# Performance work log

Hardware: AMD Instinct MI355X
Metric: run time of the kernel (lower is better)

The kernel has to match this reference:

```python
import jax, jax.numpy as jnp
import numpy as np

B, T, S, SYM, FFT = 256, 4, 2, 14, 128   # batch, num_tx, streams_per_tx, ofdm symbols, fft size
NSC, GUARD = 108, 10                      # effective subcarriers, guard offset
L = SYM * NSC                             # 1512, de-mash matrix dimension


def setup_inputs() -> dict:
    key = jax.random.key(0)
    k1, k2, k3, k4 = jax.random.split(key, 4)
    scale = 1.0 / np.sqrt(L).astype(np.float32)  # keep C roughly unitary-scaled
    return {
        "x_real": jax.random.normal(k1, (B, T, S, SYM, FFT), jnp.float32),
        "x_imag": jax.random.normal(k2, (B, T, S, SYM, FFT), jnp.float32),
        "C_real": jax.random.normal(k3, (L, L), jnp.float32) * scale,
        "C_imag": jax.random.normal(k4, (L, L), jnp.float32) * scale,
        "sc_ind": jnp.arange(NSC, dtype=jnp.int32) + GUARD,  # effective subcarrier indices
    }


def reference(x_real, x_imag, C_real, C_imag, sc_ind):
    # Complex RG and de-mash matrix
    x = jax.lax.complex(x_real, x_imag)           # [B,T,S,SYM,FFT] complex64
    C = jax.lax.complex(C_real, C_imag)           # [L,L] complex64

    # gather effective subcarriers along last axis
    y = jnp.take(x, sc_ind, axis=-1)              # [B,T,S,SYM,NSC]
    b, t, s, sym, nsc = y.shape

    # flatten_last_dims(y, 2) and multiply from right by C^H (adjoint=True)
    yf = y.reshape(b, t, s, sym * nsc)            # [B,T,S,L]
    yf = jnp.einsum('btsl,ml->btsm', yf, jnp.conj(C))  # y @ C^H
    y = yf.reshape(b, t, s, sym, nsc)             # [B,T,S,SYM,NSC]

    # scatter back into the full grid (equivalent to the transpose/scatter_nd/transpose chain,
    # since sc_ind is unique and the scatter is along the subcarrier axis)
    out = jnp.zeros(x.shape, x.dtype).at[..., sc_ind].set(y)

    # return real/imag stacked so the output is a single float32 array
    return jnp.stack([out.real, out.imag], axis=0)  # [2,B,T,S,SYM,FFT]
```

## Files before the change

kernel.cpp:

```cpp
#include <hip/hip_runtime.h>
#include <cstdint>
#include <cstddef>


typedef _Float16 half_t;
typedef half_t half8 __attribute__((ext_vector_type(8)));
typedef half_t half4 __attribute__((ext_vector_type(4)));
typedef half_t half2_t __attribute__((ext_vector_type(2)));
typedef float floatx4 __attribute__((ext_vector_type(4)));
typedef float floatv4 __attribute__((ext_vector_type(4)));

#define M_DIM 2048
#define K_DIM 3072
#define L_PAD 1536
#define N2_DIM 1536
#define LDIM 1512
#define NSC 108
#define SYMS 14
#define FFT 128
#define ROWLEN (SYMS * FFT)

#define BM 64
#define BN 64
#define BK 64
#define NITER (L_PAD / BK)

#define PA2_BLOCKS 6048
#define PW2_BLOCKS 4608
#define PAP_BLOCKS 48
#define PG_BLOCKS 4480
#define PREP_BLOCKS (PA2_BLOCKS + PW2_BLOCKS + PAP_BLOCKS + PG_BLOCKS)

typedef __attribute__((address_space(3))) uint32_t lds_u32_t;
typedef const __attribute__((address_space(1))) uint32_t glob_u32_t;

__device__ __forceinline__ void gl2lds16(const void* g, void* l) {
    __builtin_amdgcn_global_load_lds((glob_u32_t*)g, (lds_u32_t*)l, 16, 0, 0);
}

__global__ __launch_bounds__(256) void prep_all(
    const float* __restrict__ xr, const float* __restrict__ xi,
    const float* __restrict__ Cr, const float* __restrict__ Ci,
    const int* __restrict__ sc,
    half_t* __restrict__ A, half_t* __restrict__ W, float* __restrict__ out)
{
    const int b = blockIdx.x;
    const int t = threadIdx.x;

    if (b < PA2_BLOCKS) {
        int idx = b * 256 + t;
        int jp = idx % 54;
        int rest = idx / 54;
        int sym = rest % 14;
        int row = rest / 14;
        int s0 = sc[2 * jp];
        int s1 = sc[2 * jp + 1];
        const float* xrp = xr + (size_t)row * ROWLEN + sym * FFT;
        const float* xip = xi + (size_t)row * ROWLEN + sym * FFT;
        half2_t hr = { (half_t)xrp[s0], (half_t)xrp[s1] };
        half2_t hi = { (half_t)xip[s0], (half_t)xip[s1] };
        size_t dst = (size_t)row * K_DIM + sym * NSC + 2 * jp;
        *(half2_t*)(A + dst) = hr;
        *(half2_t*)(A + dst + L_PAD) = hi;
    } else if (b < PA2_BLOCKS + PW2_BLOCKS) {
        int idx = (b - PA2_BLOCKS) * 256 + t;
        int kq = idx % 768;
        int n = idx / 768;
        int k0 = kq * 4;
        floatv4 f = {0.0f, 0.0f, 0.0f, 0.0f};
        if (n < LDIM) {
            if (k0 < L_PAD) {
                if (k0 < LDIM)
                    f = *(const floatv4*)(Cr + (size_t)n * LDIM + k0);
            } else {
                int l = k0 - L_PAD;
                if (l < LDIM)
                    f = *(const floatv4*)(Ci + (size_t)n * LDIM + l);
            }
        }
        half4 h = { (half_t)f.x, (half_t)f.y, (half_t)f.z, (half_t)f.w };
        *(half4*)(W + (size_t)n * K_DIM + k0) = h;
    } else if (b < PA2_BLOCKS + PW2_BLOCKS + PAP_BLOCKS) {
        int idx = (b - PA2_BLOCKS - PW2_BLOCKS) * 256 + t;
        int c = idx % 6;
        int row = idx / 6;
        int col = (c < 3) ? (LDIM + c * 8) : (L_PAD + LDIM + (c - 3) * 8);
        half8 z = {};
        *(half8*)(A + (size_t)row * K_DIM + col) = z;
    } else {
        int idx = (b - PA2_BLOCKS - PW2_BLOCKS - PAP_BLOCKS) * 256 + t;
        int c20 = idx % 20;
        int rest = idx / 20;
        int sym = rest % 14;
        int rowri = rest / 14;
        int col = (c20 < 10) ? c20 : (NSC + c20);
        out[(size_t)rowri * ROWLEN + sym * FFT + col] = 0.0f;
    }
}

__global__ __launch_bounds__(256, 3) void gemm_scatter(
    const half_t* __restrict__ A,
    const half_t* __restrict__ W,
    const int* __restrict__ sc,
    float* __restrict__ out)
{
    __shared__ __align__(16) half_t As[BM * 2 * BK];
    __shared__ __align__(16) half_t Ws[BN * 2 * BK];

    const int t = threadIdx.x;
    const int bn = blockIdx.x;
    const int bm = blockIdx.y;
    const int lane = t & 63;
    const int w = t >> 6;
    const int wm = (w >> 1) * 32;
    const int wn = (w & 1) * 32;

    floatx4 aRR[2][2] = {}, aII[2][2] = {}, aIR[2][2] = {}, aRI[2][2] = {};

    const half_t* gA[4];
    const half_t* gW[4];
    half_t* lA[4];
    half_t* lW[4];
#pragma unroll
    for (int r = 0; r < 4; ++r) {
        int c = r * 256 + t;
        int row = c >> 4, slot = c & 15;
        int g = slot ^ (row & 15);
        int gcol = (g < 8) ? g * 8 : (L_PAD + (g - 8) * 8);
        gA[r] = A + (size_t)(bm * BM + row) * K_DIM + gcol;
        lA[r] = As + c * 8;
        gW[r] = W + (size_t)(bn * BN + row) * K_DIM + gcol;
        lW[r] = Ws + c * 8;
    }

    const int fr = lane & 15;
    const int cr = lane >> 4;

    for (int kb = 0; kb < NITER; ++kb) {
        __syncthreads();
#pragma unroll
        for (int r = 0; r < 4; ++r) gl2lds16(gA[r], lA[r]);
#pragma unroll
        for (int r = 0; r < 4; ++r) gl2lds16(gW[r], lW[r]);
#pragma unroll
        for (int r = 0; r < 4; ++r) { gA[r] += BK; gW[r] += BK; }
        __syncthreads();

#pragma unroll
        for (int ss = 0; ss < 2; ++ss) {
            const int sR = ((ss * 4 + cr) ^ fr) * 8;
            const int sI = ((8 + ss * 4 + cr) ^ fr) * 8;
            half8 yr[2], yi[2], cR[2], cI[2];
#pragma unroll
            for (int i = 0; i < 2; ++i) {
                int rb = (wm + i * 16 + fr) * (2 * BK);
                yr[i] = *(const half8*)&As[rb + sR];
                yi[i] = *(const half8*)&As[rb + sI];
            }
#pragma unroll
            for (int j = 0; j < 2; ++j) {
                int rb = (wn + j * 16 + fr) * (2 * BK);
                cR[j] = *(const half8*)&Ws[rb + sR];
                cI[j] = *(const half8*)&Ws[rb + sI];
            }
#pragma unroll
            for (int i = 0; i < 2; ++i)
#pragma unroll
                for (int j = 0; j < 2; ++j) {
                    aRR[i][j] = __builtin_amdgcn_mfma_f32_16x16x32_f16(
                        yr[i], cR[j], aRR[i][j], 0, 0, 0);
                    aII[i][j] = __builtin_amdgcn_mfma_f32_16x16x32_f16(
                        yi[i], cI[j], aII[i][j], 0, 0, 0);
                    aIR[i][j] = __builtin_amdgcn_mfma_f32_16x16x32_f16(
                        yi[i], cR[j], aIR[i][j], 0, 0, 0);
                    aRI[i][j] = __builtin_amdgcn_mfma_f32_16x16x32_f16(
                        yr[i], cI[j], aRI[i][j], 0, 0, 0);
                }
        }
    }

    const int rq = lane >> 4;
#pragma unroll
    for (int j = 0; j < 2; ++j) {
        int n = bn * BN + wn + j * 16 + fr;
        if (n >= LDIM) continue;
        int sym = n / NSC;
        int jj = n - sym * NSC;
        size_t colR = (size_t)sym * FFT + sc[jj];
        size_t colI = (size_t)M_DIM * ROWLEN + colR;
#pragma unroll
        for (int i = 0; i < 2; ++i) {
            int m0 = bm * BM + wm + i * 16 + rq * 4;
#pragma unroll
            for (int r = 0; r < 4; ++r) {
                float vr = aRR[i][j][r] + aII[i][j][r];
                float vi = aIR[i][j][r] - aRI[i][j][r];
                out[colR + (size_t)(m0 + r) * ROWLEN] = vr;
                out[colI + (size_t)(m0 + r) * ROWLEN] = vi;
            }
        }
    }
}

extern "C" void kernel_launch(void* const* d_in, const int* in_sizes, int n_in,
                              void* d_out, int out_size, void* d_ws, size_t ws_size,
                              hipStream_t stream) {
    const float* xr = (const float*)d_in[0];
    const float* xi = (const float*)d_in[1];
    const float* Cr = (const float*)d_in[2];
    const float* Ci = (const float*)d_in[3];
    const int* sc   = (const int*)d_in[4];
    float* out = (float*)d_out;

    half_t* Ah = (half_t*)d_ws;
    half_t* Wh = (half_t*)((char*)d_ws + (size_t)M_DIM * K_DIM * 2);

    prep_all<<<PREP_BLOCKS, 256, 0, stream>>>(
        xr, xi, Cr, Ci, sc, Ah, Wh, out);

    dim3 grid(N2_DIM / BN, M_DIM / BM);
    gemm_scatter<<<grid, 256, 0, stream>>>(Ah, Wh, sc, out);
}
```

Before: 144.7 us.

## Double-buffer GEMM LDS tiles with 2-wave blocks and halved K step

Restructures the complex GEMM main loop to double-buffer LDS. The next K tile is prefetched via global_load_lds while MFMAs run on the current one, and only one barrier is kept per iteration. Blocks shrink from 4 to 2 waves, each wave computing a 32x64 tile with more accumulators, and BK drops to 32 with a matching 8-slot XOR swizzle. This hides global load latency, at the cost of fewer waves per block, higher register pressure and twice as many loop iterations.

```diff
diff --git a/kernel.cpp b/kernel.cpp
--- a/kernel.cpp
+++ b/kernel.cpp
@@ -22,7 +22,7 @@
 
 #define BM 64
 #define BN 64
-#define BK 64
+#define BK 32
 #define NITER (L_PAD / BK)
 
 #define PA2_BLOCKS 6048
@@ -98,91 +98,95 @@
     }
 }
 
-__global__ __launch_bounds__(256, 3) void gemm_scatter(
+__global__ __launch_bounds__(128, 2) void gemm_scatter(
     const half_t* __restrict__ A,
     const half_t* __restrict__ W,
     const int* __restrict__ sc,
     float* __restrict__ out)
 {
-    __shared__ __align__(16) half_t As[BM * 2 * BK];
-    __shared__ __align__(16) half_t Ws[BN * 2 * BK];
+    __shared__ __align__(16) half_t As[2][BM * 2 * BK];
+    __shared__ __align__(16) half_t Ws[2][BN * 2 * BK];
 
     const int t = threadIdx.x;
     const int bn = blockIdx.x;
     const int bm = blockIdx.y;
     const int lane = t & 63;
     const int w = t >> 6;
-    const int wm = (w >> 1) * 32;
-    const int wn = (w & 1) * 32;
-
-    floatx4 aRR[2][2] = {}, aII[2][2] = {}, aIR[2][2] = {}, aRI[2][2] = {};
+    const int wm = w * 32;
+
+    floatx4 aRR[2][4] = {}, aII[2][4] = {}, aIR[2][4] = {}, aRI[2][4] = {};
 
     const half_t* gA[4];
     const half_t* gW[4];
-    half_t* lA[4];
-    half_t* lW[4];
+    int lOff[4];
 #pragma unroll
     for (int r = 0; r < 4; ++r) {
-        int c = r * 256 + t;
-        int row = c >> 4, slot = c & 15;
-        int g = slot ^ (row & 15);
-        int gcol = (g < 8) ? g * 8 : (L_PAD + (g - 8) * 8);
+        int c = r * 128 + t;
+        int row = c >> 3, slot = c & 7;
+        int g = slot ^ (row & 7);
+        int gcol = (g < 4) ? g * 8 : (L_PAD + (g - 4) * 8);
         gA[r] = A + (size_t)(bm * BM + row) * K_DIM + gcol;
-        lA[r] = As + c * 8;
         gW[r] = W + (size_t)(bn * BN + row) * K_DIM + gcol;
-        lW[r] = Ws + c * 8;
+        lOff[r] = c * 8;
     }
 
     const int fr = lane & 15;
     const int cr = lane >> 4;
+    const int sR = ((cr ^ (fr & 7))) * 8;
+    const int sI = (((4 + cr) ^ (fr & 7))) * 8;
+
+#pragma unroll
+    for (int r = 0; r < 4; ++r) {
+        gl2lds16(gA[r], &As[0][lOff[r]]);
+        gl2lds16(gW[r], &Ws[0][lOff[r]]);
+        gA[r] += BK; gW[r] += BK;
+    }
+    __syncthreads();
 
     for (int kb = 0; kb < NITER; ++kb) {
+        const int nb = kb & 1;
+        if (kb < NITER - 1) {
+#pragma unroll
+            for (int r = 0; r < 4; ++r) {
+                gl2lds16(gA[r], &As[nb ^ 1][lOff[r]]);
+                gl2lds16(gW[r], &Ws[nb ^ 1][lOff[r]]);
+                gA[r] += BK; gW[r] += BK;
+            }
+        }
+
+        half8 yr[2], yi[2], cRf[4], cIf[4];
+#pragma unroll
+        for (int i = 0; i < 2; ++i) {
+            const half_t* rb = &As[nb][(wm + i * 16 + fr) * (2 * BK)];
+            yr[i] = *(const half8*)(rb + sR);
+            yi[i] = *(const half8*)(rb + sI);
+        }
+#pragma unroll
+        for (int j = 0; j < 4; ++j) {
+            const half_t* rb = &Ws[nb][(j * 16 + fr) * (2 * BK)];
+            cRf[j] = *(const half8*)(rb + sR);
+            cIf[j] = *(const half8*)(rb + sI);
+        }
+#pragma unroll
+        for (int i = 0; i < 2; ++i)
+#pragma unroll
+            for (int j = 0; j < 4; ++j) {
+                aRR[i][j] = __builtin_amdgcn_mfma_f32_16x16x32_f16(
+                    yr[i], cRf[j], aRR[i][j], 0, 0, 0);
+                aII[i][j] = __builtin_amdgcn_mfma_f32_16x16x32_f16(
+                    yi[i], cIf[j], aII[i][j], 0, 0, 0);
+                aIR[i][j] = __builtin_amdgcn_mfma_f32_16x16x32_f16(
+                    yi[i], cRf[j], aIR[i][j], 0, 0, 0);
+                aRI[i][j] = __builtin_amdgcn_mfma_f32_16x16x32_f16(
+                    yr[i], cIf[j], aRI[i][j], 0, 0, 0);
+            }
         __syncthreads();
-#pragma unroll
-        for (int r = 0; r < 4; ++r) gl2lds16(gA[r], lA[r]);
-#pragma unroll
-        for (int r = 0; r < 4; ++r) gl2lds16(gW[r], lW[r]);
-#pragma unroll
-        for (int r = 0; r < 4; ++r) { gA[r] += BK; gW[r] += BK; }
-        __syncthreads();
-
-#pragma unroll
-        for (int ss = 0; ss < 2; ++ss) {
-            const int sR = ((ss * 4 + cr) ^ fr) * 8;
-            const int sI = ((8 + ss * 4 + cr) ^ fr) * 8;
-            half8 yr[2], yi[2], cR[2], cI[2];
-#pragma unroll
-            for (int i = 0; i < 2; ++i) {
-                int rb = (wm + i * 16 + fr) * (2 * BK);
-                yr[i] = *(const half8*)&As[rb + sR];
-                yi[i] = *(const half8*)&As[rb + sI];
-            }
-#pragma unroll
-            for (int j = 0; j < 2; ++j) {
-                int rb = (wn + j * 16 + fr) * (2 * BK);
-                cR[j] = *(const half8*)&Ws[rb + sR];
-                cI[j] = *(const half8*)&Ws[rb + sI];
-            }
-#pragma unroll
-            for (int i = 0; i < 2; ++i)
-#pragma unroll
-                for (int j = 0; j < 2; ++j) {
-                    aRR[i][j] = __builtin_amdgcn_mfma_f32_16x16x32_f16(
-                        yr[i], cR[j], aRR[i][j], 0, 0, 0);
-                    aII[i][j] = __builtin_amdgcn_mfma_f32_16x16x32_f16(
-                        yi[i], cI[j], aII[i][j], 0, 0, 0);
-                    aIR[i][j] = __builtin_amdgcn_mfma_f32_16x16x32_f16(
-                        yi[i], cR[j], aIR[i][j], 0, 0, 0);
-                    aRI[i][j] = __builtin_amdgcn_mfma_f32_16x16x32_f16(
-                        yr[i], cI[j], aRI[i][j], 0, 0, 0);
-                }
-        }
     }
 
     const int rq = lane >> 4;
 #pragma unroll
-    for (int j = 0; j < 2; ++j) {
-        int n = bn * BN + wn + j * 16 + fr;
+    for (int j = 0; j < 4; ++j) {
+        int n = bn * BN + j * 16 + fr;
         if (n >= LDIM) continue;
         int sym = n / NSC;
         int jj = n - sym * NSC;
@@ -219,5 +223,5 @@
         xr, xi, Cr, Ci, sc, Ah, Wh, out);
 
     dim3 grid(N2_DIM / BN, M_DIM / BM);
-    gemm_scatter<<<grid, 256, 0, stream>>>(Ah, Wh, sc, out);
-}
+    gemm_scatter<<<grid, 128, 0, stream>>>(Ah, Wh, sc, out);
+}
```

Result: slower. 156.3 us (+8.0%).

## Load W fragments directly from global into registers and remap block order

Applied to the files above, without the earlier changes.

The W tile no longer goes through LDS. Each wave loads its own W fragments straight from global memory into registers, which halves the LDS footprint and removes the matching LDS reads. The grid becomes a 1D launch of 768 blocks with a custom mapping that groups blocks sharing A rows and W columns, aiming for better L2 reuse. The cost is that the two row-pair waves in a block now fetch the same W data redundantly from global/L2, and the direct loads are not overlapped with compute beyond what the compiler schedules.

```diff
diff --git a/kernel.cpp b/kernel.cpp
--- a/kernel.cpp
+++ b/kernel.cpp
@@ -105,11 +105,11 @@
     float* __restrict__ out)
 {
     __shared__ __align__(16) half_t As[BM * 2 * BK];
-    __shared__ __align__(16) half_t Ws[BN * 2 * BK];
 
     const int t = threadIdx.x;
-    const int bn = blockIdx.x;
-    const int bm = blockIdx.y;
+    const int bid = blockIdx.x;
+    const int bn = (bid & 7) * 3 + ((bid >> 3) >> 5);
+    const int bm = (bid >> 3) & 31;
     const int lane = t & 63;
     const int w = t >> 6;
     const int wm = (w >> 1) * 32;
@@ -118,9 +118,7 @@
     floatx4 aRR[2][2] = {}, aII[2][2] = {}, aIR[2][2] = {}, aRI[2][2] = {};
 
     const half_t* gA[4];
-    const half_t* gW[4];
-    half_t* lA[4];
-    half_t* lW[4];
+    int lOff[4];
 #pragma unroll
     for (int r = 0; r < 4; ++r) {
         int c = r * 256 + t;
@@ -128,53 +126,62 @@
         int g = slot ^ (row & 15);
         int gcol = (g < 8) ? g * 8 : (L_PAD + (g - 8) * 8);
         gA[r] = A + (size_t)(bm * BM + row) * K_DIM + gcol;
-        lA[r] = As + c * 8;
-        gW[r] = W + (size_t)(bn * BN + row) * K_DIM + gcol;
-        lW[r] = Ws + c * 8;
+        lOff[r] = c * 8;
     }
 
     const int fr = lane & 15;
     const int cr = lane >> 4;
 
+    const half_t* wrow[2];
+#pragma unroll
+    for (int j = 0; j < 2; ++j)
+        wrow[j] = W + (size_t)(bn * BN + wn + j * 16 + fr) * K_DIM + cr * 8;
+
+#pragma unroll 1
     for (int kb = 0; kb < NITER; ++kb) {
         __syncthreads();
 #pragma unroll
-        for (int r = 0; r < 4; ++r) gl2lds16(gA[r], lA[r]);
-#pragma unroll
-        for (int r = 0; r < 4; ++r) gl2lds16(gW[r], lW[r]);
-#pragma unroll
-        for (int r = 0; r < 4; ++r) { gA[r] += BK; gW[r] += BK; }
+        for (int r = 0; r < 4; ++r) {
+            gl2lds16(gA[r], &As[lOff[r]]);
+            gA[r] += BK;
+        }
+        half8 cRf[2][2], cIf[2][2];
+#pragma unroll
+        for (int ss = 0; ss < 2; ++ss)
+#pragma unroll
+            for (int j = 0; j < 2; ++j) {
+                const half_t* p = wrow[j] + ss * 32;
+                cRf[ss][j] = *(const half8*)p;
+                cIf[ss][j] = *(const half8*)(p + L_PAD);
+            }
+#pragma unroll
+        for (int j = 0; j < 2; ++j) wrow[j] += BK;
+
         __syncthreads();
 
 #pragma unroll
         for (int ss = 0; ss < 2; ++ss) {
             const int sR = ((ss * 4 + cr) ^ fr) * 8;
             const int sI = ((8 + ss * 4 + cr) ^ fr) * 8;
-            half8 yr[2], yi[2], cR[2], cI[2];
+            half8 yr[2], yi[2];
 #pragma unroll
             for (int i = 0; i < 2; ++i) {
-                int rb = (wm + i * 16 + fr) * (2 * BK);
-                yr[i] = *(const half8*)&As[rb + sR];
-                yi[i] = *(const half8*)&As[rb + sI];
-            }
-#pragma unroll
-            for (int j = 0; j < 2; ++j) {
-                int rb = (wn + j * 16 + fr) * (2 * BK);
-                cR[j] = *(const half8*)&Ws[rb + sR];
-                cI[j] = *(const half8*)&Ws[rb + sI];
+                const half_t* rb = &As[(wm + i * 16 + fr) * (2 * BK)];
+                yr[i] = *(const half8*)(rb + sR);
+                yi[i] = *(const half8*)(rb + sI);
             }
 #pragma unroll
             for (int i = 0; i < 2; ++i)
 #pragma unroll
                 for (int j = 0; j < 2; ++j) {
                     aRR[i][j] = __builtin_amdgcn_mfma_f32_16x16x32_f16(
-                        yr[i], cR[j], aRR[i][j], 0, 0, 0);
+                        yr[i], cRf[ss][j], aRR[i][j], 0, 0, 0);
                     aII[i][j] = __builtin_amdgcn_mfma_f32_16x16x32_f16(
-                        yi[i], cI[j], aII[i][j], 0, 0, 0);
+                        yi[i], cIf[ss][j], aII[i][j], 0, 0, 0);
                     aIR[i][j] = __builtin_amdgcn_mfma_f32_16x16x32_f16(
-                        yi[i], cR[j], aIR[i][j], 0, 0, 0);
+                        yi[i], cRf[ss][j], aIR[i][j], 0, 0, 0);
                     aRI[i][j] = __builtin_amdgcn_mfma_f32_16x16x32_f16(
-                        yr[i], cI[j], aRI[i][j], 0, 0, 0);
+                        yr[i], cIf[ss][j], aRI[i][j], 0, 0, 0);
                 }
         }
     }
@@ -218,6 +225,5 @@
     prep_all<<<PREP_BLOCKS, 256, 0, stream>>>(
         xr, xi, Cr, Ci, sc, Ah, Wh, out);
 
-    dim3 grid(N2_DIM / BN, M_DIM / BM);
-    gemm_scatter<<<grid, 256, 0, stream>>>(Ah, Wh, sc, out);
-}
+    gemm_scatter<<<768, 256, 0, stream>>>(Ah, Wh, sc, out);
+}
```

After: 188.7 us. 30.5% more time.
